# Performance work log

Hardware: AMD Instinct MI355X
Metric: run time of the kernel (lower is better)

Reference implementation:

```python
import jax, jax.numpy as jnp
import numpy as np

B, LP, LR = 16, 128, 1024
D = 128
DG = 640  # 5 * 128 concat
K = 7     # number of FC trans heads
EDGE_P = 0.05


def _gcn_block(x, adj, mask, W1, b1, W2, b2):
    # x: [B,L,DG], adj: [B,L,L] (nonzero => edge weight 1, like dense_to_sparse + GCNConv)
    A = (adj != 0).astype(x.dtype)
    L = A.shape[-1]
    eye = jnp.eye(L, dtype=x.dtype)
    Ah = jnp.maximum(A, eye)                     # add_remaining_self_loops
    deg = Ah.sum(axis=1)                         # col degree [B,L] (gcn_norm uses target index)
    dinv = jax.lax.rsqrt(deg)                    # deg >= 1 thanks to self loops
    N = Ah * dinv[:, :, None] * dinv[:, None, :] # normalized adjacency per edge (r,c)
    agg = lambda h: jnp.einsum('brc,brd->bcd', N, h)  # aggregate sources r into target c
    h1 = jax.nn.relu(agg(x @ W1) + b1)
    h2 = agg(h1 @ W2) + b2
    return jax.nn.relu(x + h2) * mask[..., None]


def _fc_trans(feature, Wt, bt):
    # feature: [B,L,DG]; Wt: [K,D,DG]; bt: [K,D]
    h = jnp.einsum('bld,kod->kblo', feature, Wt) + bt[:, None, None, :]
    h = jax.nn.relu(h)                 # FCNet [640->128], ReLU (dropout off in eval)
    return jnp.swapaxes(h, 2, 3)       # [K,B,D,L] (transpose(1,2))


def _forward(x_pep, x_ss_pep, x_2_pep, x_dense_pep, x_pretrain_pep,
             x_pro, x_ss_pro, x_2_pro, x_dense_pro, x_pretrain_pro,
             x_edge_pep, x_edge_pro, x_seqmask_pep, x_seqmask_pro,
             E_seq, E_ss, E_two, W_dpep, b_dpep, W_dpro, b_dpro,
             W_ppep, b_ppep, W_ppro, b_ppro,
             Wg_pep1, bg_pep1, Wg_pep2, bg_pep2,
             Wg_pro1, bg_pro1, Wg_pro2, bg_pro2,
             Wt_pep, bt_pep, Wt_pro, bt_pro):
    enc_pep = jnp.concatenate([
        E_seq[x_pep], E_ss[x_ss_pep], E_two[x_2_pep],
        x_dense_pep @ W_dpep + b_dpep,
        x_pretrain_pep @ W_ppep + b_ppep], axis=-1) * x_seqmask_pep[..., None]
    enc_pro = jnp.concatenate([
        E_seq[x_pro], E_ss[x_ss_pro], E_two[x_2_pro],
        x_dense_pro @ W_dpro + b_dpro,
        x_pretrain_pro @ W_ppro + b_ppro], axis=-1) * x_seqmask_pro[..., None]

    f_pep = _gcn_block(enc_pep, x_edge_pep, x_seqmask_pep, Wg_pep1, bg_pep1, Wg_pep2, bg_pep2)
    f_pro = _gcn_block(enc_pro, x_edge_pro, x_seqmask_pro, Wg_pro1, bg_pro1, Wg_pro2, bg_pro2)

    pep_vecs = _fc_trans(f_pep, Wt_pep, bt_pep)[..., None]        # [K,B,D,LP,1] (unsqueeze 3)
    pro_vecs = _fc_trans(f_pro, Wt_pro, bt_pro)[:, :, :, None, :]  # [K,B,D,1,LR] (unsqueeze 2)
    return pep_vecs, pro_vecs


def setup_inputs() -> dict:
    key = jax.random.key(0)
    ks = jax.random.split(key, 40)
    f32 = jnp.float32
    s = 0.05
    inp = {
        'x_pep': jax.random.randint(ks[0], (B, LP), 0, 25),
        'x_ss_pep': jax.random.randint(ks[1], (B, LP), 0, 73),
        'x_2_pep': jax.random.randint(ks[2], (B, LP), 0, 8),
        'x_dense_pep': jax.random.normal(ks[3], (B, LP, 3), f32),
        'x_pretrain_pep': jax.random.normal(ks[4], (B, LP, 1024), f32),
        'x_pro': jax.random.randint(ks[5], (B, LR), 0, 25),
        'x_ss_pro': jax.random.randint(ks[6], (B, LR), 0, 73),
        'x_2_pro': jax.random.randint(ks[7], (B, LR), 0, 8),
        'x_dense_pro': jax.random.normal(ks[8], (B, LR, 23), f32),
        'x_pretrain_pro': jax.random.normal(ks[9], (B, LR, 1024), f32),
        'x_edge_pep': (jax.random.uniform(ks[10], (B, LP, LP)) < EDGE_P).astype(f32),
        'x_edge_pro': (jax.random.uniform(ks[11], (B, LR, LR)) < EDGE_P).astype(f32),
        'x_seqmask_pep': jnp.ones((B, LP), f32),
        'x_seqmask_pro': jnp.ones((B, LR), f32),
        'E_seq': jax.random.normal(ks[12], (25, D), f32) * s,
        'E_ss': jax.random.normal(ks[13], (73, D), f32) * s,
        'E_two': jax.random.normal(ks[14], (8, D), f32) * s,
        'W_dpep': jax.random.normal(ks[15], (3, D), f32) * s,
        'b_dpep': jnp.zeros((D,), f32),
        'W_dpro': jax.random.normal(ks[16], (23, D), f32) * s,
        'b_dpro': jnp.zeros((D,), f32),
        'W_ppep': jax.random.normal(ks[17], (1024, D), f32) * s,
        'b_ppep': jnp.zeros((D,), f32),
        'W_ppro': jax.random.normal(ks[18], (1024, D), f32) * s,
        'b_ppro': jnp.zeros((D,), f32),
        'Wg_pep1': jax.random.normal(ks[19], (DG, DG), f32) * s,
        'bg_pep1': jnp.zeros((DG,), f32),
        'Wg_pep2': jax.random.normal(ks[20], (DG, DG), f32) * s,
        'bg_pep2': jnp.zeros((DG,), f32),
        'Wg_pro1': jax.random.normal(ks[21], (DG, DG), f32) * s,
        'bg_pro1': jnp.zeros((DG,), f32),
        'Wg_pro2': jax.random.normal(ks[22], (DG, DG), f32) * s,
        'bg_pro2': jnp.zeros((DG,), f32),
        'Wt_pep': jax.random.normal(ks[23], (K, D, DG), f32) * s,
        'bt_pep': jnp.zeros((K, D), f32),
        'Wt_pro': jax.random.normal(ks[24], (K, D, DG), f32) * s,
        'bt_pro': jnp.zeros((K, D), f32),
    }
    return inp


def reference(x_pep, x_ss_pep, x_2_pep, x_dense_pep, x_pretrain_pep,
              x_pro, x_ss_pro, x_2_pro, x_dense_pro, x_pretrain_pro,
              x_edge_pep, x_edge_pro, x_seqmask_pep, x_seqmask_pro,
              E_seq, E_ss, E_two, W_dpep, b_dpep, W_dpro, b_dpro,
              W_ppep, b_ppep, W_ppro, b_ppro,
              Wg_pep1, bg_pep1, Wg_pep2, bg_pep2,
              Wg_pro1, bg_pro1, Wg_pro2, bg_pro2,
              Wt_pep, bt_pep, Wt_pro, bt_pro):
    return _forward(x_pep, x_ss_pep, x_2_pep, x_dense_pep, x_pretrain_pep,
                    x_pro, x_ss_pro, x_2_pro, x_dense_pro, x_pretrain_pro,
                    x_edge_pep, x_edge_pro, x_seqmask_pep, x_seqmask_pro,
                    E_seq, E_ss, E_two, W_dpep, b_dpep, W_dpro, b_dpro,
                    W_ppep, b_ppep, W_ppro, b_ppro,
                    Wg_pep1, bg_pep1, Wg_pep2, bg_pep2,
                    Wg_pro1, bg_pro1, Wg_pro2, bg_pro2,
                    Wt_pep, bt_pep, Wt_pro, bt_pro)
```

## Files before the change

### kernel.cpp

```cpp
#include <hip/hip_runtime.h>
#include <hip/hip_bf16.h>

#define BSZ 16
#define LP 128
#define LR 1024
#define DD 128
#define DG 640
#define KH 7
#define SPLITK 4

typedef __bf16 bf16x8 __attribute__((ext_vector_type(8)));
typedef __bf16 bf16x4v __attribute__((ext_vector_type(4)));
typedef float f32x4 __attribute__((ext_vector_type(4)));
typedef unsigned int uint32;

__device__ __forceinline__ void mfma_core_n64(
    const ushort* __restrict__ Ab, int lda,
    const ushort* __restrict__ Bb, int ldb,
    int m0, int n0, int kStart, int kEnd, f32x4 (&acc)[2][4]) {
  __shared__ __align__(16) ushort As[128 * 72];
  __shared__ __align__(16) ushort Bs[64 * 72];
  int t = threadIdx.x;
  int wave = t >> 6, lane = t & 63;
  int quad = lane >> 4, l16 = lane & 15;
  int wm = wave * 32;
  int r1 = t >> 2, o1 = (t & 3) * 16;

  int4 a0, a1, a2, a3, bb0, bb1;
  auto load_k = [&](int k0) {
    a0 = *(const int4*)(Ab + (size_t)(m0 + r1) * lda + k0 + o1);
    a1 = *(const int4*)(Ab + (size_t)(m0 + r1) * lda + k0 + o1 + 8);
    a2 = *(const int4*)(Ab + (size_t)(m0 + r1 + 64) * lda + k0 + o1);
    a3 = *(const int4*)(Ab + (size_t)(m0 + r1 + 64) * lda + k0 + o1 + 8);
    bb0 = *(const int4*)(Bb + (size_t)(n0 + r1) * ldb + k0 + o1);
    bb1 = *(const int4*)(Bb + (size_t)(n0 + r1) * ldb + k0 + o1 + 8);
  };

  load_k(kStart);
  for (int k0 = kStart; k0 < kEnd; k0 += 64) {
    __syncthreads();
    *(int4*)&As[r1 * 72 + o1] = a0;
    *(int4*)&As[r1 * 72 + o1 + 8] = a1;
    *(int4*)&As[(r1 + 64) * 72 + o1] = a2;
    *(int4*)&As[(r1 + 64) * 72 + o1 + 8] = a3;
    *(int4*)&Bs[r1 * 72 + o1] = bb0;
    *(int4*)&Bs[r1 * 72 + o1 + 8] = bb1;
    __syncthreads();
    if (k0 + 64 < kEnd) load_k(k0 + 64);
    #pragma unroll
    for (int kc = 0; kc < 2; ++kc) {
      bf16x8 af[2], bfr[4];
      #pragma unroll
      for (int fi = 0; fi < 2; ++fi)
        af[fi] = *(const bf16x8*)&As[(wm + fi * 16 + l16) * 72 + kc * 32 + quad * 8];
      #pragma unroll
      for (int fj = 0; fj < 4; ++fj)
        bfr[fj] = *(const bf16x8*)&Bs[(fj * 16 + l16) * 72 + kc * 32 + quad * 8];
      #pragma unroll
      for (int fi = 0; fi < 2; ++fi)
        #pragma unroll
        for (int fj = 0; fj < 4; ++fj)
          acc[fi][fj] = __builtin_amdgcn_mfma_f32_16x16x32_bf16(
              af[fi], bfr[fj], acc[fi][fj], 0, 0, 0);
    }
  }
}

__device__ __forceinline__ void agg_core_n64(
    const uint32* __restrict__ pb, int L,
    const ushort* __restrict__ Bb, int ldb,
    int m0, int n0, f32x4 (&acc)[2][4]) {
  __shared__ __align__(16) ushort Bs[64 * 72];
  __shared__ uint32 Aw[2][128];
  int t = threadIdx.x;
  int wave = t >> 6, lane = t & 63;
  int quad = lane >> 4, l16 = lane & 15;
  int wm = wave * 32;
  int r1 = t >> 2, o1 = (t & 3) * 16;
  int half = t >> 7, cc = t & 127;

  int4 bb0, bb1;
  uint32 w;
  auto load_k = [&](int k0) {
    bb0 = *(const int4*)(Bb + (size_t)(n0 + r1) * ldb + k0 + o1);
    bb1 = *(const int4*)(Bb + (size_t)(n0 + r1) * ldb + k0 + o1 + 8);
    w = pb[(size_t)((k0 >> 5) + half) * L + m0 + cc];
  };

  load_k(0);
  for (int k0 = 0; k0 < L; k0 += 64) {
    __syncthreads();
    *(int4*)&Bs[r1 * 72 + o1] = bb0;
    *(int4*)&Bs[r1 * 72 + o1 + 8] = bb1;
    Aw[half][cc] = w;
    __syncthreads();
    if (k0 + 64 < L) load_k(k0 + 64);
    #pragma unroll
    for (int kc = 0; kc < 2; ++kc) {
      bf16x8 af[2], bfr[4];
      #pragma unroll
      for (int fj = 0; fj < 4; ++fj)
        bfr[fj] = *(const bf16x8*)&Bs[(fj * 16 + l16) * 72 + kc * 32 + quad * 8];
      #pragma unroll
      for (int fi = 0; fi < 2; ++fi) {
        uint32 bits = (Aw[kc][wm + fi * 16 + l16] >> (quad * 8)) & 0xffu;
        int4 p;
        p.x = (int)((((bits >> 0) & 1) ? 0x3F80u : 0u) | (((bits >> 1) & 1) ? 0x3F800000u : 0u));
        p.y = (int)((((bits >> 2) & 1) ? 0x3F80u : 0u) | (((bits >> 3) & 1) ? 0x3F800000u : 0u));
        p.z = (int)((((bits >> 4) & 1) ? 0x3F80u : 0u) | (((bits >> 5) & 1) ? 0x3F800000u : 0u));
        p.w = (int)((((bits >> 6) & 1) ? 0x3F80u : 0u) | (((bits >> 7) & 1) ? 0x3F800000u : 0u));
        af[fi] = *(bf16x8*)&p;
      }
      #pragma unroll
      for (int fi = 0; fi < 2; ++fi)
        #pragma unroll
        for (int fj = 0; fj < 4; ++fj)
          acc[fi][fj] = __builtin_amdgcn_mfma_f32_16x16x32_bf16(
              af[fi], bfr[fj], acc[fi][fj], 0, 0, 0);
    }
  }
}

__device__ __forceinline__ void mfma_core_f32(
    const float* __restrict__ Af, int lda,
    const ushort* __restrict__ Bb, int ldb,
    int m0, int n0, int kStart, int kEnd, f32x4 (&acc)[4][4]) {
  __shared__ __align__(16) ushort As[128 * 72];
  __shared__ __align__(16) ushort Bs[128 * 72];
  int t = threadIdx.x;
  int wave = t >> 6, lane = t & 63;
  int quad = lane >> 4, l16 = lane & 15;
  int wm = (wave >> 1) * 64, wn = (wave & 1) * 64;
  int r1 = t >> 2, o1 = (t & 3) * 16;

  int4 b00, b01, b10, b11;
  float4 af32[8];

  auto load_k = [&](int k0) {
    b00 = *(const int4*)(Bb + (size_t)(n0 + r1) * ldb + k0 + o1);
    b01 = *(const int4*)(Bb + (size_t)(n0 + r1) * ldb + k0 + o1 + 8);
    b10 = *(const int4*)(Bb + (size_t)(n0 + r1 + 64) * ldb + k0 + o1);
    b11 = *(const int4*)(Bb + (size_t)(n0 + r1 + 64) * ldb + k0 + o1 + 8);
    #pragma unroll
    for (int s = 0; s < 8; ++s) {
      int idx = t + s * 256;
      int row = idx >> 4, c4 = (idx & 15) * 4;
      af32[s] = *(const float4*)(Af + (size_t)(m0 + row) * lda + k0 + c4);
    }
  };

  load_k(kStart);
  for (int k0 = kStart; k0 < kEnd; k0 += 64) {
    __syncthreads();
    #pragma unroll
    for (int s = 0; s < 8; ++s) {
      int idx = t + s * 256;
      int row = idx >> 4, c4 = (idx & 15) * 4;
      ushort4 u; __bf16 h;
      h = (__bf16)af32[s].x; u.x = *(ushort*)&h;
      h = (__bf16)af32[s].y; u.y = *(ushort*)&h;
      h = (__bf16)af32[s].z; u.z = *(ushort*)&h;
      h = (__bf16)af32[s].w; u.w = *(ushort*)&h;
      *(ushort4*)&As[row * 72 + c4] = u;
    }
    *(int4*)&Bs[r1 * 72 + o1] = b00;
    *(int4*)&Bs[r1 * 72 + o1 + 8] = b01;
    *(int4*)&Bs[(r1 + 64) * 72 + o1] = b10;
    *(int4*)&Bs[(r1 + 64) * 72 + o1 + 8] = b11;
    __syncthreads();
    if (k0 + 64 < kEnd) load_k(k0 + 64);
    #pragma unroll
    for (int kc = 0; kc < 2; ++kc) {
      bf16x8 af[4], bfr[4];
      #pragma unroll
      for (int fi = 0; fi < 4; ++fi)
        af[fi] = *(const bf16x8*)&As[(wm + fi * 16 + l16) * 72 + kc * 32 + quad * 8];
      #pragma unroll
      for (int fj = 0; fj < 4; ++fj)
        bfr[fj] = *(const bf16x8*)&Bs[(wn + fj * 16 + l16) * 72 + kc * 32 + quad * 8];
      #pragma unroll
      for (int fi = 0; fi < 4; ++fi)
        #pragma unroll
        for (int fj = 0; fj < 4; ++fj)
          acc[fi][fj] = __builtin_amdgcn_mfma_f32_16x16x32_bf16(
              af[fi], bfr[fj], acc[fi][fj], 0, 0, 0);
    }
  }
}

__device__ __forceinline__ void tr_tile(const float* __restrict__ src,
                                        __bf16* __restrict__ dst,
                                        int R, int C, int cb, int rb, int t) {
  __shared__ float T[32][33];
  int r0 = rb * 32, c0 = cb * 32;
  #pragma unroll
  for (int s = 0; s < 4; ++s) {
    int idx = t + s * 256;
    int r = idx >> 5, c = idx & 31;
    T[r][c] = src[(size_t)(r0 + r) * C + c0 + c];
  }
  __syncthreads();
  #pragma unroll
  for (int s = 0; s < 4; ++s) {
    int idx = t + s * 256;
    int c = idx >> 5, r = idx & 31;
    dst[(size_t)(c0 + c) * R + r0 + r] = (__bf16)T[r][c];
  }
}

__global__ __launch_bounds__(256) void prep_weights(
    const float* __restrict__ Wppep, const float* __restrict__ Wppro,
    const float* __restrict__ Wg1p, const float* __restrict__ Wg2p,
    const float* __restrict__ Wg1r, const float* __restrict__ Wg2r,
    const float* __restrict__ Wtp, const float* __restrict__ Wtr,
    __bf16* __restrict__ WppTp, __bf16* __restrict__ WppTr,
    __bf16* __restrict__ Wg1Tp, __bf16* __restrict__ Wg2Tp,
    __bf16* __restrict__ Wg1Tr, __bf16* __restrict__ Wg2Tr,
    __bf16* __restrict__ WtBp, __bf16* __restrict__ WtBr) {
  int z = blockIdx.z, bx = blockIdx.x, t = threadIdx.x;
  if (z < 2) {
    if (bx >= 128) return;
    tr_tile(z ? Wppro : Wppep, z ? WppTr : WppTp, 1024, 128, bx % 4, bx / 4, t);
  } else if (z < 6) {
    if (bx >= 400) return;
    const float* src = (z == 2) ? Wg1p : (z == 3) ? Wg2p : (z == 4) ? Wg1r : Wg2r;
    __bf16* dst = (z == 2) ? Wg1Tp : (z == 3) ? Wg2Tp : (z == 4) ? Wg1Tr : Wg2Tr;
    tr_tile(src, dst, 640, 640, bx % 20, bx / 20, t);
  } else {
    if (bx >= 560) return;
    const float* src = (z == 6) ? Wtp : Wtr;
    __bf16* dst = (z == 6) ? WtBp : WtBr;
    int i = bx * 256 + t;
    float4 v = ((const float4*)src)[i];
    bf16x4v o;
    o.x = (__bf16)v.x; o.y = (__bf16)v.y; o.z = (__bf16)v.z; o.w = (__bf16)v.w;
    ((bf16x4v*)dst)[i] = o;
  }
}

__global__ __launch_bounds__(256) void zero_f32(float* __restrict__ p, int n) {
  int i = blockIdx.x * 256 + threadIdx.x;
  if (i < n) p[i] = 0.f;
}

__global__ __launch_bounds__(256) void rsqrt_k(const float* __restrict__ deg,
                                               float* __restrict__ dinv, int n) {
  int i = blockIdx.x * 256 + threadIdx.x;
  if (i < n) dinv[i] = rsqrtf(deg[i]);
}

__global__ __launch_bounds__(256) void prep_pack_merged(
    const float* __restrict__ adjP, const float* __restrict__ adjR,
    uint32* __restrict__ packedP, uint32* __restrict__ packedR,
    float* __restrict__ degP, float* __restrict__ degR) {
  int t = threadIdx.x;
  const float* adj; uint32* packed; float* deg;
  int b, rw, c, L;
  if (blockIdx.z < 16) {
    L = LR; b = blockIdx.z; rw = blockIdx.y; c = blockIdx.x * 256 + t;
    adj = adjR; packed = packedR; deg = degR;
  } else {
    L = LP; b = blockIdx.y; rw = blockIdx.x; c = t;
    if (b >= 16 || c >= LP) return;
    adj = adjP; packed = packedP; deg = degP;
  }
  const float* adjB = adj + (size_t)b * L * L;
  uint32 w = 0;
  int rbase = rw * 32;
  #pragma unroll 8
  for (int j = 0; j < 32; ++j) {
    float a = adjB[(size_t)(rbase + j) * L + c];
    if (a != 0.f || (rbase + j) == c) w |= (1u << j);
  }
  packed[((size_t)b * (L >> 5) + rw) * L + c] = w;
  atomicAdd(deg + b * L + c, (float)__popc(w));
}

__global__ __launch_bounds__(256) void pre_gemm(
    const float* __restrict__ XpP, const float* __restrict__ XpR,
    const __bf16* __restrict__ WppTp, const __bf16* __restrict__ WppTr,
    float* __restrict__ partP, float* __restrict__ partR) {
  int bx = blockIdx.x, s = blockIdx.y;
  int pep = bx < (BSZ * LP / 128);
  int m0 = (pep ? bx : bx - BSZ * LP / 128) * 128;
  const float* A = pep ? XpP : XpR;
  const ushort* B = (const ushort*)(pep ? WppTp : WppTr);
  int BL = pep ? BSZ * LP : BSZ * LR;
  float* part = (pep ? partP : partR) + (size_t)s * BL * DD;

  f32x4 acc[4][4];
  #pragma unroll
  for (int i = 0; i < 4; ++i)
    #pragma unroll
    for (int j = 0; j < 4; ++j) acc[i][j] = (f32x4){0.f, 0.f, 0.f, 0.f};
  mfma_core_f32(A, 1024, B, 1024, m0, 0, s * (1024 / SPLITK),
                (s + 1) * (1024 / SPLITK), acc);

  int t = threadIdx.x;
  int wave = t >> 6, lane = t & 63;
  int quad = lane >> 4, l16 = lane & 15;
  int wm = (wave >> 1) * 64, wn = (wave & 1) * 64;
  #pragma unroll
  for (int fi = 0; fi < 4; ++fi)
    #pragma unroll
    for (int r = 0; r < 4; ++r) {
      int m = m0 + wm + fi * 16 + quad * 4 + r;
      #pragma unroll
      for (int fj = 0; fj < 4; ++fj) {
        int n = wn + fj * 16 + l16;
        part[(size_t)m * DD + n] = acc[fi][fj][r];
      }
    }
}

__global__ __launch_bounds__(128) void encoder_merged(
    const int* __restrict__ xsP, const int* __restrict__ xssP,
    const int* __restrict__ x2P, const float* __restrict__ xdP,
    const float* __restrict__ WdP, const float* __restrict__ bdP,
    const float* __restrict__ maskP, const float* __restrict__ partP,
    const float* __restrict__ bppP, __bf16* __restrict__ encP,
    const int* __restrict__ xsR, const int* __restrict__ xssR,
    const int* __restrict__ x2R, const float* __restrict__ xdR,
    const float* __restrict__ WdR, const float* __restrict__ bdR,
    const float* __restrict__ maskR, const float* __restrict__ partR,
    const float* __restrict__ bppR, __bf16* __restrict__ encR,
    const float* __restrict__ Eseq, const float* __restrict__ Ess,
    const float* __restrict__ Etwo) {
  int gw = blockIdx.x;
  int t = threadIdx.x;
  int pep = gw < BSZ * LP;
  int row = pep ? gw : gw - BSZ * LP;
  int BL = pep ? BSZ * LP : BSZ * LR;
  int Kd = pep ? 3 : 23;
  const int* xs = pep ? xsP : xsR;
  const int* xss = pep ? xssP : xssR;
  const int* x2 = pep ? x2P : x2R;
  const float* xd = pep ? xdP : xdR;
  const float* Wd = pep ? WdP : WdR;
  const float* bd = pep ? bdP : bdR;
  const float* mask = pep ? maskP : maskR;
  const float* part = pep ? partP : partR;
  const float* bpp = pep ? bppP : bppR;
  __bf16* enc = pep ? encP : encR;

  float m = mask[row];
  int i0 = xs[row], i1 = xss[row], i2 = x2[row];
  __bf16* e = enc + (size_t)row * DG;
  e[t]        = (__bf16)(Eseq[i0 * DD + t] * m);
  e[DD + t]   = (__bf16)(Ess[i1 * DD + t] * m);
  e[2*DD + t] = (__bf16)(Etwo[i2 * DD + t] * m);
  float acc = bd[t];
  const float* xr = xd + (size_t)row * Kd;
  for (int i = 0; i < Kd; ++i) acc = fmaf(xr[i], Wd[i * DD + t], acc);
  e[3*DD + t] = (__bf16)(acc * m);
  float p = bpp[t];
  #pragma unroll
  for (int s = 0; s < SPLITK; ++s)
    p += part[(size_t)s * BL * DD + (size_t)row * DD + t];
  e[4*DD + t] = (__bf16)(p * m);
}

__global__ __launch_bounds__(256) void linT_merged(
    const __bf16* __restrict__ WgTp, const __bf16* __restrict__ srcP,
    const float* __restrict__ dinvP, __bf16* __restrict__ dstP,
    const __bf16* __restrict__ WgTr, const __bf16* __restrict__ srcR,
    const float* __restrict__ dinvR, __bf16* __restrict__ dstR) {
  int bx = blockIdx.x;
  int pep = bx < (BSZ * LP / 64);
  int n0 = (pep ? bx : bx - BSZ * LP / 64) * 64;
  int m0 = blockIdx.y * 128;
  int BL = pep ? BSZ * LP : BSZ * LR;
  const ushort* A = (const ushort*)(pep ? WgTp : WgTr);
  const ushort* B = (const ushort*)(pep ? srcP : srcR);
  const float* dinv = pep ? dinvP : dinvR;
  __bf16* dst = pep ? dstP : dstR;

  f32x4 acc[2][4];
  #pragma unroll
  for (int i = 0; i < 2; ++i)
    #pragma unroll
    for (int j = 0; j < 4; ++j) acc[i][j] = (f32x4){0.f, 0.f, 0.f, 0.f};
  mfma_core_n64(A, DG, B, DG, m0, n0, 0, DG, acc);

  int t = threadIdx.x;
  int wave = t >> 6, lane = t & 63;
  int quad = lane >> 4, l16 = lane & 15;
  int wm = wave * 32;
  #pragma unroll
  for (int fi = 0; fi < 2; ++fi)
    #pragma unroll
    for (int r = 0; r < 4; ++r) {
      int m = m0 + wm + fi * 16 + quad * 4 + r;
      #pragma unroll
      for (int fj = 0; fj < 4; ++fj) {
        int n = n0 + fj * 16 + l16;
        dst[(size_t)m * BL + n] = (__bf16)(acc[fi][fj][r] * dinv[n]);
      }
    }
}

__global__ __launch_bounds__(256) void agg_merged(
    const uint32* __restrict__ packedP, const __bf16* __restrict__ XtP,
    const float* __restrict__ dinvP, const float* __restrict__ biasP,
    const __bf16* __restrict__ encEP, const float* __restrict__ maskP,
    __bf16* __restrict__ YP,
    const uint32* __restrict__ packedR, const __bf16* __restrict__ XtR,
    const float* __restrict__ dinvR, const float* __restrict__ biasR,
    const __bf16* __restrict__ encER, const float* __restrict__ maskR,
    __bf16* __restrict__ YR) {
  int bx = blockIdx.x;
  int b = bx / 10;
  int n0 = (bx % 10) * 64;
  int pep = (blockIdx.y == 0);
  int L = pep ? LP : LR;
  int BL = BSZ * L;
  int m0 = pep ? 0 : (blockIdx.y - 1) * 128;
  const uint32* pb = (pep ? packedP : packedR) + (size_t)b * (L >> 5) * L;
  const ushort* Bb = (const ushort*)(pep ? XtP : XtR) + (size_t)b * L;
  const float* dinv = pep ? dinvP : dinvR;
  const float* bias = pep ? biasP : biasR;
  const __bf16* encE = pep ? encEP : encER;
  const float* mask = pep ? maskP : maskR;
  __bf16* Y = pep ? YP : YR;

  f32x4 acc[2][4];
  #pragma unroll
  for (int i = 0; i < 2; ++i)
    #pragma unroll
    for (int j = 0; j < 4; ++j) acc[i][j] = (f32x4){0.f, 0.f, 0.f, 0.f};
  agg_core_n64(pb, L, Bb, BL, m0, n0, acc);

  int t = threadIdx.x;
  int wave = t >> 6, lane = t & 63;
  int quad = lane >> 4, l16 = lane & 15;
  int wm = wave * 32;
  int gRow = b * L;
  #pragma unroll
  for (int fi = 0; fi < 2; ++fi)
    #pragma unroll
    for (int r = 0; r < 4; ++r) {
      int m = m0 + wm + fi * 16 + quad * 4 + r;
      int gi = gRow + m;
      float di = dinv[gi];
      float rm = mask ? mask[gi] : 1.f;
      #pragma unroll
      for (int fj = 0; fj < 4; ++fj) {
        int n = n0 + fj * 16 + l16;
        float v = acc[fi][fj][r] * di + bias[n];
        if (encE) v += (float)encE[(size_t)gi * DG + n];
        v = fmaxf(v, 0.f);
        v *= rm;
        Y[(size_t)gi * DG + n] = (__bf16)v;
      }
    }
}

__global__ __launch_bounds__(256) void fct_merged(
    const __bf16* __restrict__ WtBp, const float* __restrict__ btp,
    const __bf16* __restrict__ Yp, float* __restrict__ outP,
    const __bf16* __restrict__ WtBr, const float* __restrict__ btr,
    const __bf16* __restrict__ Yr, float* __restrict__ outR) {
  int kh = blockIdx.y;
  int pro = (blockIdx.z < 16);
  const ushort* A;
  const ushort* B;
  const float* bt;
  int n0;
  if (pro) {
    A = (const ushort*)(WtBr + (size_t)kh * DD * DG);
    B = (const ushort*)(Yr + (size_t)blockIdx.z * LR * DG);
    bt = btr;
    n0 = blockIdx.x * 64;
  } else {
    A = (const ushort*)(WtBp + (size_t)kh * DD * DG);
    B = (const ushort*)Yp;
    bt = btp;
    n0 = ((blockIdx.z - 16) * 16 + blockIdx.x) * 64;
  }

  f32x4 acc[2][4];
  #pragma unroll
  for (int i = 0; i < 2; ++i)
    #pragma unroll
    for (int j = 0; j < 4; ++j) acc[i][j] = (f32x4){0.f, 0.f, 0.f, 0.f};
  mfma_core_n64(A, DG, B, DG, 0, n0, 0, DG, acc);

  int t = threadIdx.x;
  int wave = t >> 6, lane = t & 63;
  int quad = lane >> 4, l16 = lane & 15;
  int wm = wave * 32;
  #pragma unroll
  for (int fi = 0; fi < 2; ++fi)
    #pragma unroll
    for (int r = 0; r < 4; ++r) {
      int m = wm + fi * 16 + quad * 4 + r;
      float bb = bt[kh * DD + m];
      #pragma unroll
      for (int fj = 0; fj < 4; ++fj) {
        int n = n0 + fj * 16 + l16;
        float v = fmaxf(acc[fi][fj][r] + bb, 0.f);
        if (pro) {
          outR[((size_t)(kh * BSZ + blockIdx.z) * DD + m) * LR + n] = v;
        } else {
          int b = n >> 7, l = n & 127;
          outP[((size_t)(kh * BSZ + b) * DD + m) * LP + l] = v;
        }
      }
    }
}

extern "C" void kernel_launch(void* const* d_in, const int* in_sizes, int n_in,
                              void* d_out, int out_size, void* d_ws, size_t ws_size,
                              hipStream_t stream) {
  const int*   x_pep          = (const int*)d_in[0];
  const int*   x_ss_pep       = (const int*)d_in[1];
  const int*   x_2_pep        = (const int*)d_in[2];
  const float* x_dense_pep    = (const float*)d_in[3];
  const float* x_pretrain_pep = (const float*)d_in[4];
  const int*   x_pro          = (const int*)d_in[5];
  const int*   x_ss_pro       = (const int*)d_in[6];
  const int*   x_2_pro        = (const int*)d_in[7];
  const float* x_dense_pro    = (const float*)d_in[8];
  const float* x_pretrain_pro = (const float*)d_in[9];
  const float* x_edge_pep     = (const float*)d_in[10];
  const float* x_edge_pro     = (const float*)d_in[11];
  const float* mask_pep       = (const float*)d_in[12];
  const float* mask_pro       = (const float*)d_in[13];
  const float* E_seq          = (const float*)d_in[14];
  const float* E_ss           = (const float*)d_in[15];
  const float* E_two          = (const float*)d_in[16];
  const float* W_dpep         = (const float*)d_in[17];
  const float* b_dpep         = (const float*)d_in[18];
  const float* W_dpro         = (const float*)d_in[19];
  const float* b_dpro         = (const float*)d_in[20];
  const float* W_ppep         = (const float*)d_in[21];
  const float* b_ppep         = (const float*)d_in[22];
  const float* W_ppro         = (const float*)d_in[23];
  const float* b_ppro         = (const float*)d_in[24];
  const float* Wg_pep1        = (const float*)d_in[25];
  const float* bg_pep1        = (const float*)d_in[26];
  const float* Wg_pep2        = (const float*)d_in[27];
  const float* bg_pep2        = (const float*)d_in[28];
  const float* Wg_pro1        = (const float*)d_in[29];
  const float* bg_pro1        = (const float*)d_in[30];
  const float* Wg_pro2        = (const float*)d_in[31];
  const float* bg_pro2        = (const float*)d_in[32];
  const float* Wt_pep         = (const float*)d_in[33];
  const float* bt_pep         = (const float*)d_in[34];
  const float* Wt_pro         = (const float*)d_in[35];
  const float* bt_pro         = (const float*)d_in[36];

  float* out = (float*)d_out;
  const int BLp = BSZ * LP;
  const int BLr = BSZ * LR;
  const size_t out_pro_off = (size_t)KH * BSZ * DD * LP;

  char* w = (char*)d_ws;
  __bf16* encBp  = (__bf16*)w; w += (size_t)BLp * DG * 2;
  __bf16* encBr  = (__bf16*)w; w += (size_t)BLr * DG * 2;
  __bf16* bufATp = (__bf16*)w; w += (size_t)DG * BLp * 2;
  __bf16* bufATr = (__bf16*)w; w += (size_t)DG * BLr * 2;
  __bf16* bufYp  = (__bf16*)w; w += (size_t)BLp * DG * 2;
  __bf16* bufYr  = (__bf16*)w; w += (size_t)BLr * DG * 2;
  __bf16* WppTp  = (__bf16*)w; w += (size_t)DD * 1024 * 2;
  __bf16* WppTr  = (__bf16*)w; w += (size_t)DD * 1024 * 2;
  __bf16* Wg1Tp  = (__bf16*)w; w += (size_t)DG * DG * 2;
  __bf16* Wg2Tp  = (__bf16*)w; w += (size_t)DG * DG * 2;
  __bf16* Wg1Tr  = (__bf16*)w; w += (size_t)DG * DG * 2;
  __bf16* Wg2Tr  = (__bf16*)w; w += (size_t)DG * DG * 2;
  __bf16* WtBp   = (__bf16*)w; w += (size_t)KH * DD * DG * 2;
  __bf16* WtBr   = (__bf16*)w; w += (size_t)KH * DD * DG * 2;
  uint32* packedP = (uint32*)w; w += (size_t)BSZ * (LP / 32) * LP * 4;
  uint32* packedR = (uint32*)w; w += (size_t)BSZ * (LR / 32) * LR * 4;
  float* degP  = (float*)w; w += (size_t)BLp * 4;
  float* degR  = (float*)w; w += (size_t)BLr * 4;
  float* dinvP = (float*)w; w += (size_t)BLp * 4;
  float* dinvR = (float*)w; w += (size_t)BLr * 4;
  float* partP = (float*)w; w += (size_t)SPLITK * BLp * DD * 4;
  float* partR = (float*)w; w += (size_t)SPLITK * BLr * DD * 4;

  prep_weights<<<dim3(560, 1, 8), 256, 0, stream>>>(
      W_ppep, W_ppro, Wg_pep1, Wg_pep2, Wg_pro1, Wg_pro2, Wt_pep, Wt_pro,
      WppTp, WppTr, Wg1Tp, Wg2Tp, Wg1Tr, Wg2Tr, WtBp, WtBr);
  zero_f32<<<(BLp + BLr) / 256, 256, 0, stream>>>(degP, BLp + BLr);
  prep_pack_merged<<<dim3(4, 32, 17), 256, 0, stream>>>(
      x_edge_pep, x_edge_pro, packedP, packedR, degP, degR);
  rsqrt_k<<<(BLp + BLr) / 256, 256, 0, stream>>>(degP, dinvP, BLp + BLr);
  pre_gemm<<<dim3((BLp + BLr) / 128, SPLITK), 256, 0, stream>>>(
      x_pretrain_pep, x_pretrain_pro, WppTp, WppTr, partP, partR);
  encoder_merged<<<BLp + BLr, 128, 0, stream>>>(
      x_pep, x_ss_pep, x_2_pep, x_dense_pep, W_dpep, b_dpep, mask_pep, partP,
      b_ppep, encBp,
      x_pro, x_ss_pro, x_2_pro, x_dense_pro, W_dpro, b_dpro, mask_pro, partR,
      b_ppro, encBr,
      E_seq, E_ss, E_two);
  linT_merged<<<dim3((BLp + BLr) / 64, DG / 128), 256, 0, stream>>>(
      Wg1Tp, encBp, dinvP, bufATp, Wg1Tr, encBr, dinvR, bufATr);
  agg_merged<<<dim3(160, 9), 256, 0, stream>>>(
      packedP, bufATp, dinvP, bg_pep1, nullptr, nullptr, bufYp,
      packedR, bufATr, dinvR, bg_pro1, nullptr, nullptr, bufYr);
  linT_merged<<<dim3((BLp + BLr) / 64, DG / 128), 256, 0, stream>>>(
      Wg2Tp, bufYp, dinvP, bufATp, Wg2Tr, bufYr, dinvR, bufATr);
  agg_merged<<<dim3(160, 9), 256, 0, stream>>>(
      packedP, bufATp, dinvP, bg_pep2, encBp, mask_pep, bufYp,
      packedR, bufATr, dinvR, bg_pro2, encBr, mask_pro, bufYr);
  fct_merged<<<dim3(16, KH, 18), 256, 0, stream>>>(
      WtBp, bt_pep, bufYp, out,
      WtBr, bt_pro, bufYr, out + out_pro_off);
}
```

Baseline: 452.2 us.

## Load GEMM A-fragments directly from global memory and shrink pre_gemm M tile

The shared bf16 GEMM core no longer stages the A operand (weights) in LDS. Each wave loads its MFMA A fragments straight from global/L2 into registers, double-buffered across two k-steps, and only B goes through shared memory. The pretrain GEMM now uses 64-row tiles instead of 128, which doubles its block count and cuts per-thread registers and LDS. Both aim at better occupancy and fewer LDS round trips, in exchange for more uncoalesced global loads of A and more redundant B loads across blocks.

```diff
diff --git a/kernel.cpp b/kernel.cpp
--- a/kernel.cpp
+++ b/kernel.cpp
@@ -14,11 +14,10 @@
 typedef float f32x4 __attribute__((ext_vector_type(4)));
 typedef unsigned int uint32;
 
-__device__ __forceinline__ void mfma_core_n64(
+__device__ __forceinline__ void mfma_core_n64_aL2(
     const ushort* __restrict__ Ab, int lda,
     const ushort* __restrict__ Bb, int ldb,
-    int m0, int n0, int kStart, int kEnd, f32x4 (&acc)[2][4]) {
-  __shared__ __align__(16) ushort As[128 * 72];
+    int m0, int n0, int kEnd, f32x4 (&acc)[2][4]) {
   __shared__ __align__(16) ushort Bs[64 * 72];
   int t = threadIdx.x;
   int wave = t >> 6, lane = t & 63;
@@ -26,42 +25,55 @@
   int wm = wave * 32;
   int r1 = t >> 2, o1 = (t & 3) * 16;
 
-  int4 a0, a1, a2, a3, bb0, bb1;
-  auto load_k = [&](int k0) {
-    a0 = *(const int4*)(Ab + (size_t)(m0 + r1) * lda + k0 + o1);
-    a1 = *(const int4*)(Ab + (size_t)(m0 + r1) * lda + k0 + o1 + 8);
-    a2 = *(const int4*)(Ab + (size_t)(m0 + r1 + 64) * lda + k0 + o1);
-    a3 = *(const int4*)(Ab + (size_t)(m0 + r1 + 64) * lda + k0 + o1 + 8);
+  const ushort* aR0 = Ab + (size_t)(m0 + wm + l16) * lda + quad * 8;
+  const ushort* aR1 = aR0 + (size_t)16 * lda;
+
+  int4 bb0, bb1;
+  bf16x8 xa[4], ya[4];
+  auto load_b = [&](int k0) {
     bb0 = *(const int4*)(Bb + (size_t)(n0 + r1) * ldb + k0 + o1);
     bb1 = *(const int4*)(Bb + (size_t)(n0 + r1) * ldb + k0 + o1 + 8);
   };
-
-  load_k(kStart);
-  for (int k0 = kStart; k0 < kEnd; k0 += 64) {
+  auto load_a = [&](int k0, bf16x8 (&a)[4]) {
+    a[0] = *(const bf16x8*)(aR0 + k0);
+    a[1] = *(const bf16x8*)(aR0 + k0 + 32);
+    a[2] = *(const bf16x8*)(aR1 + k0);
+    a[3] = *(const bf16x8*)(aR1 + k0 + 32);
+  };
+  auto compute = [&](bf16x8 (&a)[4]) {
+    #pragma unroll
+    for (int kc = 0; kc < 2; ++kc) {
+      bf16x8 bfr[4];
+      #pragma unroll
+      for (int fj = 0; fj < 4; ++fj)
+        bfr[fj] = *(const bf16x8*)&Bs[(fj * 16 + l16) * 72 + kc * 32 + quad * 8];
+      #pragma unroll
+      for (int fj = 0; fj < 4; ++fj) {
+        acc[0][fj] = __builtin_amdgcn_mfma_f32_16x16x32_bf16(
+            a[kc], bfr[fj], acc[0][fj], 0, 0, 0);
+        acc[1][fj] = __builtin_amdgcn_mfma_f32_16x16x32_bf16(
+            a[2 + kc], bfr[fj], acc[1][fj], 0, 0, 0);
+      }
+    }
+  };
+
+  int nIter = kEnd >> 6;
+  load_b(0);
+  load_a(0, xa);
+  for (int it = 0; it < nIter; it += 2) {
     __syncthreads();
-    *(int4*)&As[r1 * 72 + o1] = a0;
-    *(int4*)&As[r1 * 72 + o1 + 8] = a1;
-    *(int4*)&As[(r1 + 64) * 72 + o1] = a2;
-    *(int4*)&As[(r1 + 64) * 72 + o1 + 8] = a3;
     *(int4*)&Bs[r1 * 72 + o1] = bb0;
     *(int4*)&Bs[r1 * 72 + o1 + 8] = bb1;
     __syncthreads();
-    if (k0 + 64 < kEnd) load_k(k0 + 64);
-    #pragma unroll
-    for (int kc = 0; kc < 2; ++kc) {
-      bf16x8 af[2], bfr[4];
-      #pragma unroll
-      for (int fi = 0; fi < 2; ++fi)
-        af[fi] = *(const bf16x8*)&As[(wm + fi * 16 + l16) * 72 + kc * 32 + quad * 8];
-      #pragma unroll
-      for (int fj = 0; fj < 4; ++fj)
-        bfr[fj] = *(const bf16x8*)&Bs[(fj * 16 + l16) * 72 + kc * 32 + quad * 8];
-      #pragma unroll
-      for (int fi = 0; fi < 2; ++fi)
-        #pragma unroll
-        for (int fj = 0; fj < 4; ++fj)
-          acc[fi][fj] = __builtin_amdgcn_mfma_f32_16x16x32_bf16(
-              af[fi], bfr[fj], acc[fi][fj], 0, 0, 0);
+    if (it + 1 < nIter) { load_b((it + 1) * 64); load_a((it + 1) * 64, ya); }
+    compute(xa);
+    if (it + 1 < nIter) {
+      __syncthreads();
+      *(int4*)&Bs[r1 * 72 + o1] = bb0;
+      *(int4*)&Bs[r1 * 72 + o1 + 8] = bb1;
+      __syncthreads();
+      if (it + 2 < nIter) { load_b((it + 2) * 64); load_a((it + 2) * 64, xa); }
+      compute(ya);
     }
   }
 }
@@ -121,28 +133,28 @@
   }
 }
 
-__device__ __forceinline__ void mfma_core_f32(
+__device__ __forceinline__ void mfma_core_f32_m64(
     const float* __restrict__ Af, int lda,
     const ushort* __restrict__ Bb, int ldb,
-    int m0, int n0, int kStart, int kEnd, f32x4 (&acc)[4][4]) {
-  __shared__ __align__(16) ushort As[128 * 72];
+    int m0, int kStart, int kEnd, f32x4 (&acc)[2][4]) {
+  __shared__ __align__(16) ushort As[64 * 72];
   __shared__ __align__(16) ushort Bs[128 * 72];
   int t = threadIdx.x;
   int wave = t >> 6, lane = t & 63;
   int quad = lane >> 4, l16 = lane & 15;
-  int wm = (wave >> 1) * 64, wn = (wave & 1) * 64;
+  int wm = (wave >> 1) * 32, wn = (wave & 1) * 64;
   int r1 = t >> 2, o1 = (t & 3) * 16;
 
   int4 b00, b01, b10, b11;
-  float4 af32[8];
+  float4 af32[4];
 
   auto load_k = [&](int k0) {
-    b00 = *(const int4*)(Bb + (size_t)(n0 + r1) * ldb + k0 + o1);
-    b01 = *(const int4*)(Bb + (size_t)(n0 + r1) * ldb + k0 + o1 + 8);
-    b10 = *(const int4*)(Bb + (size_t)(n0 + r1 + 64) * ldb + k0 + o1);
-    b11 = *(const int4*)(Bb + (size_t)(n0 + r1 + 64) * ldb + k0 + o1 + 8);
-    #pragma unroll
-    for (int s = 0; s < 8; ++s) {
+    b00 = *(const int4*)(Bb + (size_t)r1 * ldb + k0 + o1);
+    b01 = *(const int4*)(Bb + (size_t)r1 * ldb + k0 + o1 + 8);
+    b10 = *(const int4*)(Bb + (size_t)(r1 + 64) * ldb + k0 + o1);
+    b11 = *(const int4*)(Bb + (size_t)(r1 + 64) * ldb + k0 + o1 + 8);
+    #pragma unroll
+    for (int s = 0; s < 4; ++s) {
       int idx = t + s * 256;
       int row = idx >> 4, c4 = (idx & 15) * 4;
       af32[s] = *(const float4*)(Af + (size_t)(m0 + row) * lda + k0 + c4);
@@ -153,7 +165,7 @@
   for (int k0 = kStart; k0 < kEnd; k0 += 64) {
     __syncthreads();
     #pragma unroll
-    for (int s = 0; s < 8; ++s) {
+    for (int s = 0; s < 4; ++s) {
       int idx = t + s * 256;
       int row = idx >> 4, c4 = (idx & 15) * 4;
       ushort4 u; __bf16 h;
@@ -171,15 +183,15 @@
     if (k0 + 64 < kEnd) load_k(k0 + 64);
     #pragma unroll
     for (int kc = 0; kc < 2; ++kc) {
-      bf16x8 af[4], bfr[4];
-      #pragma unroll
-      for (int fi = 0; fi < 4; ++fi)
+      bf16x8 af[2], bfr[4];
+      #pragma unroll
+      for (int fi = 0; fi < 2; ++fi)
         af[fi] = *(const bf16x8*)&As[(wm + fi * 16 + l16) * 72 + kc * 32 + quad * 8];
       #pragma unroll
       for (int fj = 0; fj < 4; ++fj)
         bfr[fj] = *(const bf16x8*)&Bs[(wn + fj * 16 + l16) * 72 + kc * 32 + quad * 8];
       #pragma unroll
-      for (int fi = 0; fi < 4; ++fi)
+      for (int fi = 0; fi < 2; ++fi)
         #pragma unroll
         for (int fj = 0; fj < 4; ++fj)
           acc[fi][fj] = __builtin_amdgcn_mfma_f32_16x16x32_bf16(
@@ -281,27 +293,27 @@
     const __bf16* __restrict__ WppTp, const __bf16* __restrict__ WppTr,
     float* __restrict__ partP, float* __restrict__ partR) {
   int bx = blockIdx.x, s = blockIdx.y;
-  int pep = bx < (BSZ * LP / 128);
-  int m0 = (pep ? bx : bx - BSZ * LP / 128) * 128;
+  int pep = bx < (BSZ * LP / 64);
+  int m0 = (pep ? bx : bx - BSZ * LP / 64) * 64;
   const float* A = pep ? XpP : XpR;
   const ushort* B = (const ushort*)(pep ? WppTp : WppTr);
   int BL = pep ? BSZ * LP : BSZ * LR;
   float* part = (pep ? partP : partR) + (size_t)s * BL * DD;
 
-  f32x4 acc[4][4];
-  #pragma unroll
-  for (int i = 0; i < 4; ++i)
+  f32x4 acc[2][4];
+  #pragma unroll
+  for (int i = 0; i < 2; ++i)
     #pragma unroll
     for (int j = 0; j < 4; ++j) acc[i][j] = (f32x4){0.f, 0.f, 0.f, 0.f};
-  mfma_core_f32(A, 1024, B, 1024, m0, 0, s * (1024 / SPLITK),
-                (s + 1) * (1024 / SPLITK), acc);
+  mfma_core_f32_m64(A, 1024, B, 1024, m0, s * (1024 / SPLITK),
+                    (s + 1) * (1024 / SPLITK), acc);
 
   int t = threadIdx.x;
   int wave = t >> 6, lane = t & 63;
   int quad = lane >> 4, l16 = lane & 15;
-  int wm = (wave >> 1) * 64, wn = (wave & 1) * 64;
-  #pragma unroll
-  for (int fi = 0; fi < 4; ++fi)
+  int wm = (wave >> 1) * 32, wn = (wave & 1) * 64;
+  #pragma unroll
+  for (int fi = 0; fi < 2; ++fi)
     #pragma unroll
     for (int r = 0; r < 4; ++r) {
       int m = m0 + wm + fi * 16 + quad * 4 + r;
@@ -380,7 +392,7 @@
   for (int i = 0; i < 2; ++i)
     #pragma unroll
     for (int j = 0; j < 4; ++j) acc[i][j] = (f32x4){0.f, 0.f, 0.f, 0.f};
-  mfma_core_n64(A, DG, B, DG, m0, n0, 0, DG, acc);
+  mfma_core_n64_aL2(A, DG, B, DG, m0, n0, DG, acc);
 
   int t = threadIdx.x;
   int wave = t >> 6, lane = t & 63;
@@ -483,7 +495,7 @@
   for (int i = 0; i < 2; ++i)
     #pragma unroll
     for (int j = 0; j < 4; ++j) acc[i][j] = (f32x4){0.f, 0.f, 0.f, 0.f};
-  mfma_core_n64(A, DG, B, DG, 0, n0, 0, DG, acc);
+  mfma_core_n64_aL2(A, DG, B, DG, 0, n0, DG, acc);
 
   int t = threadIdx.x;
   int wave = t >> 6, lane = t & 63;
@@ -586,7 +598,7 @@
   prep_pack_merged<<<dim3(4, 32, 17), 256, 0, stream>>>(
       x_edge_pep, x_edge_pro, packedP, packedR, degP, degR);
   rsqrt_k<<<(BLp + BLr) / 256, 256, 0, stream>>>(degP, dinvP, BLp + BLr);
-  pre_gemm<<<dim3((BLp + BLr) / 128, SPLITK), 256, 0, stream>>>(
+  pre_gemm<<<dim3((BLp + BLr) / 64, SPLITK), 256, 0, stream>>>(
       x_pretrain_pep, x_pretrain_pro, WppTp, WppTr, partP, partR);
   encoder_merged<<<BLp + BLr, 128, 0, stream>>>(
       x_pep, x_ss_pep, x_2_pep, x_dense_pep, W_dpep, b_dpep, mask_pep, partP,
```

Result: slower. 483.8 us (+7.0%).
